# Optimization experiments

Measured on AMD Instinct MI355X. Metric: run time of the kernel, lower is better.

Reference implementation:

```python
import jax, jax.numpy as jnp
import numpy as np

B, S, D = 4, 2048, 1024
H = 16
DH = D // H  # head dim for qk and v

def setup_inputs() -> dict:
    key = jax.random.key(0)
    ks = jax.random.split(key, 5)
    x_q = jax.random.normal(ks[0], (B, S, D), dtype=jnp.float32)
    # weights stored as [d_in, d_out] (equivalent to torch Linear weight.T)
    scale = 1.0 / np.sqrt(D)
    Wq = jax.random.normal(ks[1], (D, D), dtype=jnp.float32) * scale
    Wk = jax.random.normal(ks[2], (D, D), dtype=jnp.float32) * scale
    Wv = jax.random.normal(ks[3], (D, D), dtype=jnp.float32) * scale
    Wo = jax.random.normal(ks[4], (D, D), dtype=jnp.float32) * scale
    return {"x_q": x_q, "Wq": Wq, "Wk": Wk, "Wv": Wv, "Wo": Wo}

def reference(x_q, Wq, Wk, Wv, Wo):
    b, sq, _ = x_q.shape
    sk = sq  # self-attention: x_k = x_v = x_q
    # projections -> [b, h, s, dh]
    q = (x_q @ Wq).reshape(b, sq, H, DH).transpose(0, 2, 1, 3)
    k = (x_q @ Wk).reshape(b, sk, H, DH).transpose(0, 2, 1, 3)
    v = (x_q @ Wv).reshape(b, sk, H, DH).transpose(0, 2, 1, 3)
    # scores [b, h, sq, sk]
    scores = jnp.einsum('bhqd,bhkd->bhqk', q, k)
    # causal mask: triu(ones(sq, sk), diagonal=1 + sk - sq)
    i = jnp.arange(sq)[:, None]
    j = jnp.arange(sk)[None, :]
    mask = (j - i) >= (1 + sk - sq)
    scores = jnp.where(mask, -jnp.inf, scores)
    attn = jax.nn.softmax(scores / jnp.sqrt(jnp.float32(DH)), axis=-1)
    # dropout p=0.0 -> identity
    ctx = jnp.einsum('bhqk,bhkd->bhqd', attn, v)  # [b,h,sq,dh]
    ctx = ctx.transpose(0, 2, 1, 3).reshape(b, sq, H * DH)
    return ctx @ Wo
```

## Files before the change

kernel.cpp:

```cpp
#include <hip/hip_runtime.h>

#define S_LEN 2048
#define D_MODEL 1024
#define NH 16
#define DHEAD 64
#define BATCH 4

typedef _Float16 half8 __attribute__((ext_vector_type(8)));
typedef __fp16 fp16x2 __attribute__((ext_vector_type(2)));
typedef float floatx4 __attribute__((ext_vector_type(4)));

#define EXP2SCALE 0.1803368801111244f

__device__ __forceinline__ unsigned short f2h(float f) {
    _Float16 h = (_Float16)f;
    return __builtin_bit_cast(unsigned short, h);
}

__device__ __forceinline__ float fexp2(float x) {
    float r;
    asm("v_exp_f32 %0, %1" : "=v"(r) : "v"(x));
    return r;
}
__device__ __forceinline__ float frcp(float x) {
    float r;
    asm("v_rcp_f32 %0, %1" : "=v"(r) : "v"(x));
    return r;
}

__device__ __forceinline__ unsigned int pk2(float a, float b) {
    fp16x2 p = __builtin_amdgcn_cvt_pkrtz(a, b);
    return __builtin_bit_cast(unsigned int, p);
}

__device__ __forceinline__ void gload_lds16(const unsigned short* g, unsigned short* l) {
    __builtin_amdgcn_global_load_lds(
        (const __attribute__((address_space(1))) void*)g,
        (__attribute__((address_space(3))) void*)l,
        16, 0, 0);
}

__global__ __launch_bounds__(256) void convert_f2h_kernel(const float* __restrict__ in,
                                                          unsigned short* __restrict__ out,
                                                          int n4) {
    int i = blockIdx.x * 256 + threadIdx.x;
    if (i < n4) {
        float4 v = ((const float4*)in)[i];
        ushort4 o;
        o.x = f2h(v.x); o.y = f2h(v.y); o.z = f2h(v.z); o.w = f2h(v.w);
        ((ushort4*)out)[i] = o;
    }
}

__global__ __launch_bounds__(256) void transpose_w_kernel(const float* __restrict__ W0,
                                                          const float* __restrict__ W1,
                                                          const float* __restrict__ W2,
                                                          const float* __restrict__ W3,
                                                          unsigned short* __restrict__ T0,
                                                          unsigned short* __restrict__ T1,
                                                          unsigned short* __restrict__ T2,
                                                          unsigned short* __restrict__ T3) {
    const float* W = blockIdx.z == 0 ? W0 : blockIdx.z == 1 ? W1 : blockIdx.z == 2 ? W2 : W3;
    unsigned short* Wt = blockIdx.z == 0 ? T0 : blockIdx.z == 1 ? T1 : blockIdx.z == 2 ? T2 : T3;
    __shared__ float tile[32][33];
    int x = threadIdx.x;
    int y = threadIdx.y;
    int k0 = blockIdx.y * 32;
    int n0 = blockIdx.x * 32;
    for (int i = 0; i < 4; i++)
        tile[y + 8 * i][x] = W[(size_t)(k0 + y + 8 * i) * D_MODEL + n0 + x];
    __syncthreads();
    for (int i = 0; i < 4; i++)
        Wt[(size_t)(n0 + y + 8 * i) * D_MODEL + k0 + x] = f2h(tile[x][y + 8 * i]);
}

template<int MODE>
__device__ __forceinline__ void gemm_body(const unsigned short* __restrict__ A,
                                          const unsigned short* __restrict__ Bt,
                                          void* __restrict__ Cout,
                                          int M, int N, int K,
                                          int bx, int by,
                                          unsigned short* smem, float osc) {
    const int tid  = threadIdx.x;
    const int wave = tid >> 6;
    const int lane = tid & 63;
    const int quad = lane >> 4;
    const int l16  = lane & 15;
    const int wm = (wave >> 1) * 64;
    const int wn = (wave & 1) * 64;
    const int tm = by * 128;
    const int tn = bx * 128;

    int rowi[4], gci[4];
#pragma unroll
    for (int i = 0; i < 4; i++) {
        int ci = tid + i * 256;
        rowi[i] = ci >> 3;
        gci[i]  = (ci & 7) ^ (rowi[i] & 7);
    }

    floatx4 acc[4][4] = {};

#pragma unroll
    for (int i = 0; i < 4; i++) {
        gload_lds16(A  + (size_t)(tm + rowi[i]) * K + gci[i] * 8, &smem[i * 2048 + wave * 512]);
        gload_lds16(Bt + (size_t)(tn + rowi[i]) * K + gci[i] * 8, &smem[8192 + i * 2048 + wave * 512]);
    }

    int slot = 0;
    for (int k0 = 0; k0 < K; k0 += 64) {
        __syncthreads();
        if (k0 + 64 < K) {
            unsigned short* nb = smem + (slot ^ 1) * 16384;
#pragma unroll
            for (int i = 0; i < 4; i++) {
                gload_lds16(A  + (size_t)(tm + rowi[i]) * K + (k0 + 64) + gci[i] * 8,
                            &nb[i * 2048 + wave * 512]);
                gload_lds16(Bt + (size_t)(tn + rowi[i]) * K + (k0 + 64) + gci[i] * 8,
                            &nb[8192 + i * 2048 + wave * 512]);
            }
        }
        const unsigned short* As = smem + slot * 16384;
        const unsigned short* Bs = As + 8192;

#pragma unroll
        for (int ks = 0; ks < 2; ks++) {
            half8 af[4], bf[4];
#pragma unroll
            for (int mi = 0; mi < 4; mi++) {
                int row = wm + mi * 16 + l16;
                af[mi] = *(const half8*)(&As[row * 64 + ((((ks << 2) | quad) ^ (row & 7)) << 3)]);
            }
#pragma unroll
            for (int ni = 0; ni < 4; ni++) {
                int row = wn + ni * 16 + l16;
                bf[ni] = *(const half8*)(&Bs[row * 64 + ((((ks << 2) | quad) ^ (row & 7)) << 3)]);
            }
#pragma unroll
            for (int mi = 0; mi < 4; mi++)
#pragma unroll
                for (int ni = 0; ni < 4; ni++)
                    acc[mi][ni] = __builtin_amdgcn_mfma_f32_16x16x32_f16(af[mi], bf[ni], acc[mi][ni], 0, 0, 0);
        }
        slot ^= 1;
    }

    if (MODE == 2) {
#pragma unroll
        for (int mi = 0; mi < 4; mi++)
#pragma unroll
            for (int ni = 0; ni < 4; ni++)
#pragma unroll
                for (int r = 0; r < 4; r++) {
                    int row = tm + wm + mi * 16 + quad * 4 + r;
                    int col = tn + wn + ni * 16 + l16;
                    ((float*)Cout)[(size_t)row * N + col] = acc[mi][ni][r];
                }
        return;
    }

    __syncthreads();
    if (MODE == 0) {
#pragma unroll
        for (int mi = 0; mi < 4; mi++)
#pragma unroll
            for (int ni = 0; ni < 4; ni++) {
                int col = wn + ni * 16 + l16;
                int cc  = col >> 4;
                int cil = col & 15;
#pragma unroll
                for (int r = 0; r < 4; r++) {
                    int row = wm + mi * 16 + quad * 4 + r;
                    smem[row * 128 + ((cc ^ ((row >> 2) & 7)) << 4) + cil] = f2h(acc[mi][ni][r] * osc);
                }
            }
        __syncthreads();
        unsigned short* O = (unsigned short*)Cout;
#pragma unroll
        for (int j = 0; j < 8; j++) {
            int vid = tid + j * 256;
            int row = vid >> 4, vv = vid & 15;
            int cc = vv >> 1, hf = vv & 1;
            uint4 v = *(const uint4*)(&smem[row * 128 + ((cc ^ ((row >> 2) & 7)) << 4) + hf * 8]);
            int grow = tm + row;
            int b = grow >> 11, s = grow & 2047;
            int n = tn + vv * 8;
            int h = n >> 6, dh = n & 63;
            *(uint4*)(O + (((size_t)(b * NH + h) * S_LEN + s) * DHEAD + dh)) = v;
        }
    } else {
#pragma unroll
        for (int mi = 0; mi < 4; mi++)
#pragma unroll
            for (int ni = 0; ni < 4; ni++) {
                int col = wn + ni * 16 + l16;
                int sw  = (col >> 2) & 7;
#pragma unroll
                for (int r = 0; r < 4; r++) {
                    int row = wm + mi * 16 + quad * 4 + r;
                    smem[col * 128 + (((row >> 4) ^ sw) << 4) + (row & 15)] = f2h(acc[mi][ni][r]);
                }
            }
        __syncthreads();
        unsigned short* O = (unsigned short*)Cout;
        int b = tm >> 11;
        int sbase = tm & 2047;
#pragma unroll
        for (int j = 0; j < 8; j++) {
            int vid = tid + j * 256;
            int colr = vid >> 4, vv = vid & 15;
            int rc = vv >> 1, hf = vv & 1;
            uint4 v = *(const uint4*)(&smem[colr * 128 + ((rc ^ ((colr >> 2) & 7)) << 4) + hf * 8]);
            int n = tn + colr;
            int h = n >> 6, dh = n & 63;
            *(uint4*)(O + (((size_t)(b * NH + h) * DHEAD + dh) * S_LEN + sbase + vv * 8)) = v;
        }
    }
}

__global__ __launch_bounds__(256) void qkv_gemm_kernel(const unsigned short* __restrict__ A,
                                                       const unsigned short* __restrict__ Wq,
                                                       const unsigned short* __restrict__ Wk,
                                                       const unsigned short* __restrict__ Wv,
                                                       unsigned short* __restrict__ Qo,
                                                       unsigned short* __restrict__ Ko,
                                                       unsigned short* __restrict__ Vo) {
    __shared__ unsigned short smem[2 * 16384];
    const int z = blockIdx.z;
    if (z == 2)
        gemm_body<1>(A, Wv, Vo, BATCH * S_LEN, D_MODEL, D_MODEL, blockIdx.x, blockIdx.y, smem, 1.f);
    else
        gemm_body<0>(A, z == 0 ? Wq : Wk, z == 0 ? Qo : Ko,
                     BATCH * S_LEN, D_MODEL, D_MODEL, blockIdx.x, blockIdx.y, smem,
                     z == 0 ? EXP2SCALE : 1.f);
}

__global__ __launch_bounds__(256) void out_gemm_kernel(const unsigned short* __restrict__ A,
                                                       const unsigned short* __restrict__ Bt,
                                                       float* __restrict__ C) {
    __shared__ unsigned short smem[2 * 16384];
    gemm_body<2>(A, Bt, C, BATCH * S_LEN, D_MODEL, D_MODEL, blockIdx.x, blockIdx.y, smem, 1.f);
}

__global__ __launch_bounds__(512, 4) void attn_kernel(const unsigned short* __restrict__ Q,
                                                      const unsigned short* __restrict__ K,
                                                      const unsigned short* __restrict__ Vt,
                                                      unsigned short* __restrict__ ctx) {
    __shared__ unsigned short smem[34816];
    unsigned short* Ps = smem + 16384;
    const int tid  = threadIdx.x;
    const int wave = tid >> 6;
    const int wg   = wave >> 2;
    const int wv   = wave & 3;
    const int lane = tid & 63;
    const int quad = lane >> 4;
    const int l16  = lane & 15;
    const int bx = blockIdx.x;
    const int h  = blockIdx.y;
    const int b  = blockIdx.z;
    const size_t head = (size_t)(b * NH + h) * (S_LEN * DHEAD);

    const int ta = bx, tb = 15 - bx;
    const int tw = wg ? tb : ta;
    const int rounds = 2 * tb + 2;
    const int dk  = 2 * tw + (wv >> 1);
    const int qg0 = tw * 128 + wv * 32 + l16;

    half8 qf[2][2];
#pragma unroll
    for (int s = 0; s < 2; s++)
#pragma unroll
        for (int ks = 0; ks < 2; ks++)
            qf[s][ks] = *(const half8*)(Q + head + (size_t)(qg0 + s * 16) * DHEAD + ks * 32 + quad * 8);

    const int r0 = tid >> 3;
    const int g0 = (tid & 7) ^ (r0 & 7);
    const unsigned short* pK = K  + head + (size_t)r0 * DHEAD + g0 * 8;
    const unsigned short* pV = Vt + head + (size_t)r0 * S_LEN + g0 * 8;
    const int sdst = wave * 512;

    const int akb0 = l16 * 64 + ((quad    ) ^ (l16 & 7)) * 8;
    const int akb1 = l16 * 64 + ((4 | quad) ^ (l16 & 7)) * 8;
    const int psr  = wave * 2304 + l16 * 72;

    floatx4 acc0[4] = {}, acc1[4] = {};
    float l0 = 0.f, l1 = 0.f;

    gload_lds16(pK, smem + sdst);
    gload_lds16(pV, smem + 8192 + sdst);
    pK += 64 * DHEAD; pV += 64;

    for (int c = 0; c < rounds; c++) {
        __syncthreads();
        const int cur = c & 1;
        if (c + 1 < rounds) {
            gload_lds16(pK, smem + (cur ^ 1) * 4096 + sdst);
            gload_lds16(pV, smem + 8192 + (cur ^ 1) * 4096 + sdst);
            pK += 64 * DHEAD; pV += 64;
        }
        if (c > dk) continue;

        const unsigned short* Ksb = smem + cur * 4096;
        const unsigned short* Vsb = smem + 8192 + cur * 4096;

        floatx4 sc0[4] = {}, sc1[4] = {};
#pragma unroll
        for (int ks = 0; ks < 2; ks++) {
            const int ab = ks ? akb1 : akb0;
#pragma unroll
            for (int mk = 0; mk < 4; mk++) {
                half8 ak = *(const half8*)(&Ksb[mk * 1024 + ab]);
                sc0[mk] = __builtin_amdgcn_mfma_f32_16x16x32_f16(ak, qf[0][ks], sc0[mk], 0, 0, 0);
                sc1[mk] = __builtin_amdgcn_mfma_f32_16x16x32_f16(ak, qf[1][ks], sc1[mk], 0, 0, 0);
            }
        }

        const bool diag = (c == dk);

#define SOFTMAX_SET(sc, l_s, qg, setofs)                                          \
        {                                                                         \
            if (diag) {                                                           \
                int rel = (qg) - c * 64 - quad * 4;                               \
                _Pragma("unroll")                                                 \
                for (int mk = 0; mk < 4; mk++)                                    \
                    _Pragma("unroll")                                             \
                    for (int r = 0; r < 4; r++)                                   \
                        if (mk * 16 + r > rel) sc[mk][r] = -3.0e38f;              \
            }                                                                     \
            float rs = 0.f;                                                       \
            _Pragma("unroll")                                                     \
            for (int mk = 0; mk < 4; mk++)                                        \
                _Pragma("unroll")                                                 \
                for (int r = 0; r < 4; r++) {                                     \
                    float e = fexp2(sc[mk][r]);                                   \
                    sc[mk][r] = e;                                                \
                    rs += e;                                                      \
                }                                                                 \
            rs += __shfl_xor(rs, 16, 64);                                         \
            rs += __shfl_xor(rs, 32, 64);                                         \
            l_s += rs;                                                            \
            _Pragma("unroll")                                                     \
            for (int mk = 0; mk < 4; mk++) {                                      \
                uint2 u;                                                          \
                u.x = pk2(sc[mk][0], sc[mk][1]);                                  \
                u.y = pk2(sc[mk][2], sc[mk][3]);                                  \
                *(uint2*)(&Ps[psr + (setofs) + mk * 16 + quad * 4]) = u;          \
            }                                                                     \
        }

        SOFTMAX_SET(sc0, l0, qg0,      0)
        SOFTMAX_SET(sc1, l1, qg0 + 16, 1152)
#undef SOFTMAX_SET

#pragma unroll
        for (int ks = 0; ks < 2; ks++) {
            const int ab = ks ? akb1 : akb0;
            half8 bp0 = *(const half8*)(&Ps[psr        + ks * 32 + quad * 8]);
            half8 bp1 = *(const half8*)(&Ps[psr + 1152 + ks * 32 + quad * 8]);
#pragma unroll
            for (int db = 0; db < 4; db++) {
                half8 av = *(const half8*)(&Vsb[db * 1024 + ab]);
                acc0[db] = __builtin_amdgcn_mfma_f32_16x16x32_f16(av, bp0, acc0[db], 0, 0, 0);
                acc1[db] = __builtin_amdgcn_mfma_f32_16x16x32_f16(av, bp1, acc1[db], 0, 0, 0);
            }
        }
    }

    __syncthreads();
#pragma unroll
    for (int s = 0; s < 2; s++) {
        float inv = frcp(s ? l1 : l0);
        int qrow = wg * 128 + wv * 32 + s * 16 + l16;
        floatx4* ac = s ? acc1 : acc0;
#pragma unroll
        for (int db = 0; db < 4; db++) {
            uint2 u;
            u.x = pk2(ac[db][0] * inv, ac[db][1] * inv);
            u.y = pk2(ac[db][2] * inv, ac[db][3] * inv);
            int chunk = db * 2 + (quad >> 1);
            int sw = chunk ^ (qrow & 7);
            *(uint2*)(&smem[qrow * 64 + sw * 8 + (quad & 1) * 4]) = u;
        }
    }
    __syncthreads();
#pragma unroll
    for (int j = 0; j < 4; j++) {
        int vid = j * 512 + tid;
        int ql = vid >> 3, slot = vid & 7;
        uint4 v = *(const uint4*)(&smem[ql * 64 + slot * 8]);
        int dhc = slot ^ (ql & 7);
        int q = (ql < 128 ? ta * 128 : tb * 128 - 128) + ql;
        *(uint4*)(ctx + ((size_t)b * S_LEN + q) * D_MODEL + h * DHEAD + dhc * 8) = v;
    }
}

extern "C" void kernel_launch(void* const* d_in, const int* in_sizes, int n_in,
                              void* d_out, int out_size, void* d_ws, size_t ws_size,
                              hipStream_t stream) {
    const float* x  = (const float*)d_in[0];
    const float* Wq = (const float*)d_in[1];
    const float* Wk = (const float*)d_in[2];
    const float* Wv = (const float*)d_in[3];
    const float* Wo = (const float*)d_in[4];

    char* ws = (char*)d_ws;
    unsigned short* Xh   = (unsigned short*)(ws + 0);
    unsigned short* Wqt  = (unsigned short*)(ws + 16777216);
    unsigned short* Wkt  = (unsigned short*)(ws + 18874368);
    unsigned short* Wvt  = (unsigned short*)(ws + 20971520);
    unsigned short* Wot  = (unsigned short*)(ws + 23068672);
    unsigned short* Qh   = (unsigned short*)(ws + 25165824);
    unsigned short* Kh   = (unsigned short*)(ws + 41943040);
    unsigned short* Vth  = (unsigned short*)(ws + 58720256);
    unsigned short* ctxh = (unsigned short*)(ws + 75497472);

    const int M = BATCH * S_LEN;

    convert_f2h_kernel<<<(M * D_MODEL / 4 + 255) / 256, 256, 0, stream>>>(x, Xh, M * D_MODEL / 4);
    transpose_w_kernel<<<dim3(32, 32, 4), dim3(32, 8), 0, stream>>>(Wq, Wk, Wv, Wo, Wqt, Wkt, Wvt, Wot);

    qkv_gemm_kernel<<<dim3(8, 64, 3), 256, 0, stream>>>(Xh, Wqt, Wkt, Wvt, Qh, Kh, Vth);

    attn_kernel<<<dim3(8, NH, BATCH), 512, 0, stream>>>(Qh, Kh, Vth, ctxh);

    out_gemm_kernel<<<dim3(8, 64), 256, 0, stream>>>(ctxh, Wot, (float*)d_out);
}
```

Baseline: 237.7 us.

## Replace QKV projection GEMM with 256x256-tile, 8-wave pipelined kernel

Adds a dedicated QKV GEMM kernel using 256x256 output tiles with 512 threads, double-buffered direct global-to-LDS loads interleaved with MFMA phases, and s_setprio hints, replacing the 128x128 generic gemm_body path. Larger tiles raise arithmetic intensity and cut redundant global reads of X and weights. The price is 128 KB of LDS per block and a 128-register accumulator per thread. The grid shrinks to 384 blocks, which may leave some CUs idle.

```diff
diff --git a/kernel.cpp b/kernel.cpp
--- a/kernel.cpp
+++ b/kernel.cpp
@@ -74,6 +74,219 @@
         Wt[(size_t)(n0 + y + 8 * i) * D_MODEL + k0 + x] = f2h(tile[x][y + 8 * i]);
 }
 
+__global__ __launch_bounds__(512, 2) void qkv_gemm256_kernel(const unsigned short* __restrict__ A,
+                                                             const unsigned short* __restrict__ Wq,
+                                                             const unsigned short* __restrict__ Wk,
+                                                             const unsigned short* __restrict__ Wv,
+                                                             unsigned short* __restrict__ Qo,
+                                                             unsigned short* __restrict__ Ko,
+                                                             unsigned short* __restrict__ Vo) {
+    __shared__ unsigned short smem[65536];
+    const int z = blockIdx.z;
+    const unsigned short* Bt = z == 0 ? Wq : z == 1 ? Wk : Wv;
+    unsigned short* O = z == 0 ? Qo : z == 1 ? Ko : Vo;
+    const float osc = z == 0 ? EXP2SCALE : 1.f;
+
+    const int tid  = threadIdx.x;
+    const int wave = tid >> 6;
+    const int lane = tid & 63;
+    const int quad = lane >> 4;
+    const int l16  = lane & 15;
+    const int wr   = wave >> 2;
+    const int wc   = wave & 3;
+    const int tm   = blockIdx.y * 256;
+    const int tn   = blockIdx.x * 256;
+    const int wofs = wave * 512;
+
+    const unsigned short* pAj[4];
+    const unsigned short* pBj[4];
+#pragma unroll
+    for (int j = 0; j < 4; j++) {
+        int ci = tid + j * 512;
+        int r  = ci >> 3;
+        int g  = (tid & 7) ^ (r & 7);
+        pAj[j] = A  + (size_t)(tm + r) * D_MODEL + g * 8;
+        pBj[j] = Bt + (size_t)(tn + r) * D_MODEL + g * 8;
+    }
+
+    const int sK0 = ((quad       ) ^ (l16 & 7)) << 3;
+    const int sK1 = (((4 | quad) ) ^ (l16 & 7)) << 3;
+    const int arow = wr * 128 + l16;
+    const int brow = wc * 64  + l16;
+
+    floatx4 acc[8][4] = {};
+    half8 af[4][2], bf[4][2];
+
+    {
+        unsigned short* Ab0 = smem;
+        unsigned short* Bb0 = smem + 32768;
+        gload_lds16(pBj[0], Bb0 +        wofs);
+        gload_lds16(pBj[1], Bb0 + 4096 + wofs);
+        gload_lds16(pBj[2], Bb0 + 8192 + wofs);
+        gload_lds16(pBj[3], Bb0 + 12288 + wofs);
+        gload_lds16(pAj[0], Ab0 +        wofs);
+        gload_lds16(pAj[2], Ab0 + 8192 + wofs);
+        gload_lds16(pAj[1], Ab0 + 4096 + wofs);
+        gload_lds16(pAj[3], Ab0 + 12288 + wofs);
+#pragma unroll
+        for (int j = 0; j < 4; j++) { pAj[j] += 64; pBj[j] += 64; }
+    }
+
+    for (int t = 0; t < 16; t++) {
+        const int pt = t & 1;
+        const unsigned short* Ab = smem + pt * 16384;
+        const unsigned short* Bb = smem + 32768 + pt * 16384;
+        unsigned short* An = smem + (pt ^ 1) * 16384;
+        unsigned short* Bn = smem + 32768 + (pt ^ 1) * 16384;
+
+        if (t < 15) {
+            gload_lds16(pBj[0], Bn +        wofs);
+            gload_lds16(pBj[1], Bn + 4096 + wofs);
+            asm volatile("s_waitcnt vmcnt(4)" ::: "memory");
+        } else {
+            asm volatile("s_waitcnt vmcnt(2)" ::: "memory");
+        }
+        __builtin_amdgcn_s_barrier();
+#pragma unroll
+        for (int m2 = 0; m2 < 4; m2++) {
+            int ro = (arow + m2 * 16) * 64;
+            af[m2][0] = *(const half8*)(Ab + ro + sK0);
+            af[m2][1] = *(const half8*)(Ab + ro + sK1);
+        }
+#pragma unroll
+        for (int ni = 0; ni < 2; ni++) {
+            int ro = (brow + ni * 16) * 64;
+            bf[ni][0] = *(const half8*)(Bb + ro + sK0);
+            bf[ni][1] = *(const half8*)(Bb + ro + sK1);
+        }
+        __builtin_amdgcn_s_setprio(1);
+#pragma unroll
+        for (int m2 = 0; m2 < 4; m2++)
+#pragma unroll
+            for (int ni = 0; ni < 2; ni++) {
+                acc[m2][ni] = __builtin_amdgcn_mfma_f32_16x16x32_f16(af[m2][0], bf[ni][0], acc[m2][ni], 0, 0, 0);
+                acc[m2][ni] = __builtin_amdgcn_mfma_f32_16x16x32_f16(af[m2][1], bf[ni][1], acc[m2][ni], 0, 0, 0);
+            }
+        __builtin_amdgcn_s_setprio(0);
+
+        if (t < 15) {
+            gload_lds16(pBj[2], Bn + 8192 + wofs);
+            gload_lds16(pBj[3], Bn + 12288 + wofs);
+        }
+#pragma unroll
+        for (int ni = 2; ni < 4; ni++) {
+            int ro = (brow + ni * 16) * 64;
+            bf[ni][0] = *(const half8*)(Bb + ro + sK0);
+            bf[ni][1] = *(const half8*)(Bb + ro + sK1);
+        }
+        __builtin_amdgcn_s_setprio(1);
+#pragma unroll
+        for (int m2 = 0; m2 < 4; m2++)
+#pragma unroll
+            for (int ni = 2; ni < 4; ni++) {
+                acc[m2][ni] = __builtin_amdgcn_mfma_f32_16x16x32_f16(af[m2][0], bf[ni][0], acc[m2][ni], 0, 0, 0);
+                acc[m2][ni] = __builtin_amdgcn_mfma_f32_16x16x32_f16(af[m2][1], bf[ni][1], acc[m2][ni], 0, 0, 0);
+            }
+        __builtin_amdgcn_s_setprio(0);
+
+        if (t < 15) {
+            gload_lds16(pAj[0], An +        wofs);
+            gload_lds16(pAj[2], An + 8192 + wofs);
+            asm volatile("s_waitcnt vmcnt(6)" ::: "memory");
+        } else {
+            asm volatile("s_waitcnt vmcnt(0)" ::: "memory");
+        }
+        __builtin_amdgcn_s_barrier();
+#pragma unroll
+        for (int m2 = 0; m2 < 4; m2++) {
+            int ro = (arow + 64 + m2 * 16) * 64;
+            af[m2][0] = *(const half8*)(Ab + ro + sK0);
+            af[m2][1] = *(const half8*)(Ab + ro + sK1);
+        }
+        __builtin_amdgcn_s_setprio(1);
+#pragma unroll
+        for (int m2 = 0; m2 < 4; m2++)
+#pragma unroll
+            for (int ni = 2; ni < 4; ni++) {
+                acc[4 + m2][ni] = __builtin_amdgcn_mfma_f32_16x16x32_f16(af[m2][0], bf[ni][0], acc[4 + m2][ni], 0, 0, 0);
+                acc[4 + m2][ni] = __builtin_amdgcn_mfma_f32_16x16x32_f16(af[m2][1], bf[ni][1], acc[4 + m2][ni], 0, 0, 0);
+            }
+        __builtin_amdgcn_s_setprio(0);
+
+        if (t < 15) {
+            gload_lds16(pAj[1], An + 4096 + wofs);
+            gload_lds16(pAj[3], An + 12288 + wofs);
+#pragma unroll
+            for (int j = 0; j < 4; j++) { pAj[j] += 64; pBj[j] += 64; }
+        }
+        __builtin_amdgcn_s_setprio(1);
+#pragma unroll
+        for (int m2 = 0; m2 < 4; m2++)
+#pragma unroll
+            for (int ni = 0; ni < 2; ni++) {
+                acc[4 + m2][ni] = __builtin_amdgcn_mfma_f32_16x16x32_f16(af[m2][0], bf[ni][0], acc[4 + m2][ni], 0, 0, 0);
+                acc[4 + m2][ni] = __builtin_amdgcn_mfma_f32_16x16x32_f16(af[m2][1], bf[ni][1], acc[4 + m2][ni], 0, 0, 0);
+            }
+        __builtin_amdgcn_s_setprio(0);
+    }
+
+    __syncthreads();
+
+    if (z != 2) {
+#pragma unroll
+        for (int mi = 0; mi < 8; mi++)
+#pragma unroll
+            for (int ni = 0; ni < 4; ni++) {
+                int col = wc * 64 + ni * 16 + l16;
+                int cc  = col >> 4;
+                int cil = col & 15;
+#pragma unroll
+                for (int r = 0; r < 4; r++) {
+                    int row = wr * 128 + mi * 16 + quad * 4 + r;
+                    smem[row * 256 + ((cc ^ ((row >> 2) & 15)) << 4) + cil] = f2h(acc[mi][ni][r] * osc);
+                }
+            }
+        __syncthreads();
+#pragma unroll
+        for (int j = 0; j < 16; j++) {
+            int vid = tid + j * 512;
+            int row = vid >> 5, vv = vid & 31;
+            int cc = vv >> 1, hf = vv & 1;
+            uint4 v = *(const uint4*)(&smem[row * 256 + ((cc ^ ((row >> 2) & 15)) << 4) + hf * 8]);
+            int grow = tm + row;
+            int b = grow >> 11, s = grow & 2047;
+            int n = tn + vv * 8;
+            int h = n >> 6, dh = n & 63;
+            *(uint4*)(O + (((size_t)(b * NH + h) * S_LEN + s) * DHEAD + dh)) = v;
+        }
+    } else {
+#pragma unroll
+        for (int mi = 0; mi < 8; mi++)
+#pragma unroll
+            for (int ni = 0; ni < 4; ni++) {
+                int col = wc * 64 + ni * 16 + l16;
+                int sw  = (col >> 2) & 15;
+#pragma unroll
+                for (int r = 0; r < 4; r++) {
+                    int row = wr * 128 + mi * 16 + quad * 4 + r;
+                    smem[col * 256 + (((row >> 4) ^ sw) << 4) + (row & 15)] = f2h(acc[mi][ni][r]);
+                }
+            }
+        __syncthreads();
+        int b = tm >> 11, sbase = tm & 2047;
+#pragma unroll
+        for (int j = 0; j < 16; j++) {
+            int vid = tid + j * 512;
+            int colr = vid >> 5, vv = vid & 31;
+            int rc = vv >> 1, hf = vv & 1;
+            uint4 v = *(const uint4*)(&smem[colr * 256 + ((rc ^ ((colr >> 2) & 15)) << 4) + hf * 8]);
+            int n = tn + colr;
+            int h = n >> 6, dh = n & 63;
+            *(uint4*)(O + (((size_t)(b * NH + h) * DHEAD + dh) * S_LEN + sbase + vv * 8)) = v;
+        }
+    }
+}
+
 template<int MODE>
 __device__ __forceinline__ void gemm_body(const unsigned short* __restrict__ A,
                                           const unsigned short* __restrict__ Bt,
@@ -158,81 +371,6 @@
                 }
         return;
     }
-
-    __syncthreads();
-    if (MODE == 0) {
-#pragma unroll
-        for (int mi = 0; mi < 4; mi++)
-#pragma unroll
-            for (int ni = 0; ni < 4; ni++) {
-                int col = wn + ni * 16 + l16;
-                int cc  = col >> 4;
-                int cil = col & 15;
-#pragma unroll
-                for (int r = 0; r < 4; r++) {
-                    int row = wm + mi * 16 + quad * 4 + r;
-                    smem[row * 128 + ((cc ^ ((row >> 2) & 7)) << 4) + cil] = f2h(acc[mi][ni][r] * osc);
-                }
-            }
-        __syncthreads();
-        unsigned short* O = (unsigned short*)Cout;
-#pragma unroll
-        for (int j = 0; j < 8; j++) {
-            int vid = tid + j * 256;
-            int row = vid >> 4, vv = vid & 15;
-            int cc = vv >> 1, hf = vv & 1;
-            uint4 v = *(const uint4*)(&smem[row * 128 + ((cc ^ ((row >> 2) & 7)) << 4) + hf * 8]);
-            int grow = tm + row;
-            int b = grow >> 11, s = grow & 2047;
-            int n = tn + vv * 8;
-            int h = n >> 6, dh = n & 63;
-            *(uint4*)(O + (((size_t)(b * NH + h) * S_LEN + s) * DHEAD + dh)) = v;
-        }
-    } else {
-#pragma unroll
-        for (int mi = 0; mi < 4; mi++)
-#pragma unroll
-            for (int ni = 0; ni < 4; ni++) {
-                int col = wn + ni * 16 + l16;
-                int sw  = (col >> 2) & 7;
-#pragma unroll
-                for (int r = 0; r < 4; r++) {
-                    int row = wm + mi * 16 + quad * 4 + r;
-                    smem[col * 128 + (((row >> 4) ^ sw) << 4) + (row & 15)] = f2h(acc[mi][ni][r]);
-                }
-            }
-        __syncthreads();
-        unsigned short* O = (unsigned short*)Cout;
-        int b = tm >> 11;
-        int sbase = tm & 2047;
-#pragma unroll
-        for (int j = 0; j < 8; j++) {
-            int vid = tid + j * 256;
-            int colr = vid >> 4, vv = vid & 15;
-            int rc = vv >> 1, hf = vv & 1;
-            uint4 v = *(const uint4*)(&smem[colr * 128 + ((rc ^ ((colr >> 2) & 7)) << 4) + hf * 8]);
-            int n = tn + colr;
-            int h = n >> 6, dh = n & 63;
-            *(uint4*)(O + (((size_t)(b * NH + h) * DHEAD + dh) * S_LEN + sbase + vv * 8)) = v;
-        }
-    }
-}
-
-__global__ __launch_bounds__(256) void qkv_gemm_kernel(const unsigned short* __restrict__ A,
-                                                       const unsigned short* __restrict__ Wq,
-                                                       const unsigned short* __restrict__ Wk,
-                                                       const unsigned short* __restrict__ Wv,
-                                                       unsigned short* __restrict__ Qo,
-                                                       unsigned short* __restrict__ Ko,
-                                                       unsigned short* __restrict__ Vo) {
-    __shared__ unsigned short smem[2 * 16384];
-    const int z = blockIdx.z;
-    if (z == 2)
-        gemm_body<1>(A, Wv, Vo, BATCH * S_LEN, D_MODEL, D_MODEL, blockIdx.x, blockIdx.y, smem, 1.f);
-    else
-        gemm_body<0>(A, z == 0 ? Wq : Wk, z == 0 ? Qo : Ko,
-                     BATCH * S_LEN, D_MODEL, D_MODEL, blockIdx.x, blockIdx.y, smem,
-                     z == 0 ? EXP2SCALE : 1.f);
 }
 
 __global__ __launch_bounds__(256) void out_gemm_kernel(const unsigned short* __restrict__ A,
@@ -419,7 +557,7 @@
     convert_f2h_kernel<<<(M * D_MODEL / 4 + 255) / 256, 256, 0, stream>>>(x, Xh, M * D_MODEL / 4);
     transpose_w_kernel<<<dim3(32, 32, 4), dim3(32, 8), 0, stream>>>(Wq, Wk, Wv, Wo, Wqt, Wkt, Wvt, Wot);
 
-    qkv_gemm_kernel<<<dim3(8, 64, 3), 256, 0, stream>>>(Xh, Wqt, Wkt, Wvt, Qh, Kh, Vth);
+    qkv_gemm256_kernel<<<dim3(4, 32, 3), 512, 0, stream>>>(Xh, Wqt, Wkt, Wvt, Qh, Kh, Vth);
 
     attn_kernel<<<dim3(8, NH, BATCH), 512, 0, stream>>>(Qh, Kh, Vth, ctxh);
 
```

New measurement: 230.3 us. 1.03x faster.

## Interleave GEMM prefetch with split MFMA phases and add XCD-aware block swizzle

Applied to the files above, without the earlier changes.

The GEMM main loop is restructured into four MFMA quarter-phases, with global-to-LDS prefetches placed between them. Explicit vmcnt waits, raw s_barrier and setprio replace the single __syncthreads per k-step, so loads overlap compute and fewer fragment registers are live. GEMM and attention blocks are remapped so consecutive logical tiles land on the same XCD, which is meant to improve L2 reuse, and the GEMMs get launch_bounds(256,2). The hand-tuned waitcnt counts are fragile, and the hardcoded pointer strides and trip count assume K=1024 and fixed grid sizes.

```diff
diff --git a/kernel.cpp b/kernel.cpp
--- a/kernel.cpp
+++ b/kernel.cpp
@@ -78,7 +78,7 @@
 __device__ __forceinline__ void gemm_body(const unsigned short* __restrict__ A,
                                           const unsigned short* __restrict__ Bt,
                                           void* __restrict__ Cout,
-                                          int M, int N, int K,
+                                          int N, int K,
                                           int bx, int by,
                                           unsigned short* smem, float osc) {
     const int tid  = threadIdx.x;
@@ -91,58 +91,129 @@
     const int tm = by * 128;
     const int tn = bx * 128;
 
-    int rowi[4], gci[4];
-#pragma unroll
-    for (int i = 0; i < 4; i++) {
-        int ci = tid + i * 256;
-        rowi[i] = ci >> 3;
-        gci[i]  = (ci & 7) ^ (rowi[i] & 7);
-    }
+    const int r0 = tid >> 3;
+    const int g0 = (tid & 7) ^ (r0 & 7);
+    const unsigned short* pA = A  + (size_t)(tm + r0) * K + g0 * 8;
+    const unsigned short* pB = Bt + (size_t)(tn + r0) * K + g0 * 8;
+    const int wofs = wave * 512;
+
+    const int sK0 = (((0 << 2) | quad) ^ (l16 & 7)) << 3;
+    const int sK1 = (((1 << 2) | quad) ^ (l16 & 7)) << 3;
+    const int arow = wm + l16;
+    const int brow = wn + l16;
 
     floatx4 acc[4][4] = {};
-
-#pragma unroll
-    for (int i = 0; i < 4; i++) {
-        gload_lds16(A  + (size_t)(tm + rowi[i]) * K + gci[i] * 8, &smem[i * 2048 + wave * 512]);
-        gload_lds16(Bt + (size_t)(tn + rowi[i]) * K + gci[i] * 8, &smem[8192 + i * 2048 + wave * 512]);
-    }
-
-    int slot = 0;
-    for (int k0 = 0; k0 < K; k0 += 64) {
-        __syncthreads();
-        if (k0 + 64 < K) {
-            unsigned short* nb = smem + (slot ^ 1) * 16384;
-#pragma unroll
-            for (int i = 0; i < 4; i++) {
-                gload_lds16(A  + (size_t)(tm + rowi[i]) * K + (k0 + 64) + gci[i] * 8,
-                            &nb[i * 2048 + wave * 512]);
-                gload_lds16(Bt + (size_t)(tn + rowi[i]) * K + (k0 + 64) + gci[i] * 8,
-                            &nb[8192 + i * 2048 + wave * 512]);
-            }
-        }
-        const unsigned short* As = smem + slot * 16384;
-        const unsigned short* Bs = As + 8192;
-
-#pragma unroll
-        for (int ks = 0; ks < 2; ks++) {
-            half8 af[4], bf[4];
-#pragma unroll
-            for (int mi = 0; mi < 4; mi++) {
-                int row = wm + mi * 16 + l16;
-                af[mi] = *(const half8*)(&As[row * 64 + ((((ks << 2) | quad) ^ (row & 7)) << 3)]);
-            }
-#pragma unroll
-            for (int ni = 0; ni < 4; ni++) {
-                int row = wn + ni * 16 + l16;
-                bf[ni] = *(const half8*)(&Bs[row * 64 + ((((ks << 2) | quad) ^ (row & 7)) << 3)]);
-            }
-#pragma unroll
-            for (int mi = 0; mi < 4; mi++)
-#pragma unroll
-                for (int ni = 0; ni < 4; ni++)
-                    acc[mi][ni] = __builtin_amdgcn_mfma_f32_16x16x32_f16(af[mi], bf[ni], acc[mi][ni], 0, 0, 0);
-        }
-        slot ^= 1;
+    half8 af[2][2], bf[4][2];
+
+    {
+        unsigned short* Ab = smem;
+        unsigned short* Bb = smem + 8192;
+        gload_lds16(pB,         Bb +        wofs);
+        gload_lds16(pB + 65536, Bb + 4096 + wofs);
+        gload_lds16(pB + 32768, Bb + 2048 + wofs);
+        gload_lds16(pB + 98304, Bb + 6144 + wofs);
+        gload_lds16(pA,         Ab +        wofs);
+        gload_lds16(pA + 65536, Ab + 4096 + wofs);
+        gload_lds16(pA + 32768, Ab + 2048 + wofs);
+        gload_lds16(pA + 98304, Ab + 6144 + wofs);
+        pA += 64; pB += 64;
+    }
+
+    for (int t = 0; t < 16; t++) {
+        const unsigned short* Ab = smem + (t & 1) * 16384;
+        const unsigned short* Bb = Ab + 8192;
+        unsigned short* An = smem + ((t & 1) ^ 1) * 16384;
+        unsigned short* Bn = An + 8192;
+        const bool pf = (t < 15);
+
+        if (pf) {
+            gload_lds16(pB,         Bn +        wofs);
+            gload_lds16(pB + 65536, Bn + 4096 + wofs);
+            asm volatile("s_waitcnt vmcnt(4)" ::: "memory");
+        } else {
+            asm volatile("s_waitcnt vmcnt(2)" ::: "memory");
+        }
+        __builtin_amdgcn_s_barrier();
+#pragma unroll
+        for (int m2 = 0; m2 < 2; m2++) {
+            int ro = (arow + m2 * 16) * 64;
+            af[m2][0] = *(const half8*)(Ab + ro + sK0);
+            af[m2][1] = *(const half8*)(Ab + ro + sK1);
+        }
+#pragma unroll
+        for (int ni = 0; ni < 2; ni++) {
+            int ro = (brow + ni * 16) * 64;
+            bf[ni][0] = *(const half8*)(Bb + ro + sK0);
+            bf[ni][1] = *(const half8*)(Bb + ro + sK1);
+        }
+        __builtin_amdgcn_s_setprio(1);
+#pragma unroll
+        for (int m2 = 0; m2 < 2; m2++)
+#pragma unroll
+            for (int ni = 0; ni < 2; ni++) {
+                acc[m2][ni] = __builtin_amdgcn_mfma_f32_16x16x32_f16(af[m2][0], bf[ni][0], acc[m2][ni], 0, 0, 0);
+                acc[m2][ni] = __builtin_amdgcn_mfma_f32_16x16x32_f16(af[m2][1], bf[ni][1], acc[m2][ni], 0, 0, 0);
+            }
+        __builtin_amdgcn_s_setprio(0);
+
+        if (pf) {
+            gload_lds16(pB + 32768, Bn + 2048 + wofs);
+            gload_lds16(pB + 98304, Bn + 6144 + wofs);
+        }
+#pragma unroll
+        for (int ni = 2; ni < 4; ni++) {
+            int ro = (brow + ni * 16) * 64;
+            bf[ni][0] = *(const half8*)(Bb + ro + sK0);
+            bf[ni][1] = *(const half8*)(Bb + ro + sK1);
+        }
+        __builtin_amdgcn_s_setprio(1);
+#pragma unroll
+        for (int m2 = 0; m2 < 2; m2++)
+#pragma unroll
+            for (int ni = 2; ni < 4; ni++) {
+                acc[m2][ni] = __builtin_amdgcn_mfma_f32_16x16x32_f16(af[m2][0], bf[ni][0], acc[m2][ni], 0, 0, 0);
+                acc[m2][ni] = __builtin_amdgcn_mfma_f32_16x16x32_f16(af[m2][1], bf[ni][1], acc[m2][ni], 0, 0, 0);
+            }
+        __builtin_amdgcn_s_setprio(0);
+
+        if (pf) {
+            gload_lds16(pA,         An +        wofs);
+            gload_lds16(pA + 65536, An + 4096 + wofs);
+            asm volatile("s_waitcnt vmcnt(6)" ::: "memory");
+        } else {
+            asm volatile("s_waitcnt vmcnt(0)" ::: "memory");
+        }
+        __builtin_amdgcn_s_barrier();
+#pragma unroll
+        for (int m2 = 0; m2 < 2; m2++) {
+            int ro = (arow + (2 + m2) * 16) * 64;
+            af[m2][0] = *(const half8*)(Ab + ro + sK0);
+            af[m2][1] = *(const half8*)(Ab + ro + sK1);
+        }
+        __builtin_amdgcn_s_setprio(1);
+#pragma unroll
+        for (int m2 = 0; m2 < 2; m2++)
+#pragma unroll
+            for (int ni = 2; ni < 4; ni++) {
+                acc[2 + m2][ni] = __builtin_amdgcn_mfma_f32_16x16x32_f16(af[m2][0], bf[ni][0], acc[2 + m2][ni], 0, 0, 0);
+                acc[2 + m2][ni] = __builtin_amdgcn_mfma_f32_16x16x32_f16(af[m2][1], bf[ni][1], acc[2 + m2][ni], 0, 0, 0);
+            }
+        __builtin_amdgcn_s_setprio(0);
+
+        if (pf) {
+            gload_lds16(pA + 32768, An + 2048 + wofs);
+            gload_lds16(pA + 98304, An + 6144 + wofs);
+            pA += 64; pB += 64;
+        }
+        __builtin_amdgcn_s_setprio(1);
+#pragma unroll
+        for (int m2 = 0; m2 < 2; m2++)
+#pragma unroll
+            for (int ni = 0; ni < 2; ni++) {
+                acc[2 + m2][ni] = __builtin_amdgcn_mfma_f32_16x16x32_f16(af[m2][0], bf[ni][0], acc[2 + m2][ni], 0, 0, 0);
+                acc[2 + m2][ni] = __builtin_amdgcn_mfma_f32_16x16x32_f16(af[m2][1], bf[ni][1], acc[2 + m2][ni], 0, 0, 0);
+            }
+        __builtin_amdgcn_s_setprio(0);
     }
 
     if (MODE == 2) {
@@ -218,28 +289,38 @@
     }
 }
 
-__global__ __launch_bounds__(256) void qkv_gemm_kernel(const unsigned short* __restrict__ A,
-                                                       const unsigned short* __restrict__ Wq,
-                                                       const unsigned short* __restrict__ Wk,
-                                                       const unsigned short* __restrict__ Wv,
-                                                       unsigned short* __restrict__ Qo,
-                                                       unsigned short* __restrict__ Ko,
-                                                       unsigned short* __restrict__ Vo) {
-    __shared__ unsigned short smem[2 * 16384];
+__device__ __forceinline__ void xcd_swz_512(int& bx, int& by) {
+    int lin = bx + (by << 3);
+    int nl = (lin & 7) * 64 + (lin >> 3);
+    bx = nl & 7;
+    by = nl >> 3;
+}
+
+__global__ __launch_bounds__(256, 2) void qkv_gemm_kernel(const unsigned short* __restrict__ A,
+                                                          const unsigned short* __restrict__ Wq,
+                                                          const unsigned short* __restrict__ Wk,
+                                                          const unsigned short* __restrict__ Wv,
+                                                          unsigned short* __restrict__ Qo,
+                                                          unsigned short* __restrict__ Ko,
+                                                          unsigned short* __restrict__ Vo) {
+    __shared__ unsigned short smem[32768];
+    int bx = blockIdx.x, by = blockIdx.y;
+    xcd_swz_512(bx, by);
     const int z = blockIdx.z;
     if (z == 2)
-        gemm_body<1>(A, Wv, Vo, BATCH * S_LEN, D_MODEL, D_MODEL, blockIdx.x, blockIdx.y, smem, 1.f);
+        gemm_body<1>(A, Wv, Vo, D_MODEL, D_MODEL, bx, by, smem, 1.f);
     else
         gemm_body<0>(A, z == 0 ? Wq : Wk, z == 0 ? Qo : Ko,
-                     BATCH * S_LEN, D_MODEL, D_MODEL, blockIdx.x, blockIdx.y, smem,
-                     z == 0 ? EXP2SCALE : 1.f);
-}
-
-__global__ __launch_bounds__(256) void out_gemm_kernel(const unsigned short* __restrict__ A,
-                                                       const unsigned short* __restrict__ Bt,
-                                                       float* __restrict__ C) {
-    __shared__ unsigned short smem[2 * 16384];
-    gemm_body<2>(A, Bt, C, BATCH * S_LEN, D_MODEL, D_MODEL, blockIdx.x, blockIdx.y, smem, 1.f);
+                     D_MODEL, D_MODEL, bx, by, smem, z == 0 ? EXP2SCALE : 1.f);
+}
+
+__global__ __launch_bounds__(256, 2) void out_gemm_kernel(const unsigned short* __restrict__ A,
+                                                          const unsigned short* __restrict__ Bt,
+                                                          float* __restrict__ C) {
+    __shared__ unsigned short smem[32768];
+    int bx = blockIdx.x, by = blockIdx.y;
+    xcd_swz_512(bx, by);
+    gemm_body<2>(A, Bt, C, D_MODEL, D_MODEL, bx, by, smem, 1.f);
 }
 
 __global__ __launch_bounds__(512, 4) void attn_kernel(const unsigned short* __restrict__ Q,
@@ -255,9 +336,11 @@
     const int lane = tid & 63;
     const int quad = lane >> 4;
     const int l16  = lane & 15;
-    const int bx = blockIdx.x;
-    const int h  = blockIdx.y;
-    const int b  = blockIdx.z;
+    int lin = blockIdx.x + (blockIdx.y << 3) + (blockIdx.z << 7);
+    int nl  = (lin & 7) * 64 + (lin >> 3);
+    const int bx = nl & 7;
+    const int h  = (nl >> 3) & 15;
+    const int b  = nl >> 7;
     const size_t head = (size_t)(b * NH + h) * (S_LEN * DHEAD);
 
     const int ta = bx, tb = 15 - bx;
```

Measured after the change: 226.7 us. -4.6%, faster.
